# Kernel optimization log

Hardware: AMD Instinct MI355X
Metric: run time of the kernel (lower is better)

Reference implementation:

```python
import jax, jax.numpy as jnp
import numpy as np

NEG = -1e30  # log-space 'zero' sentinel (avoids -inf NaNs in grads)
BLANK = 0


def setup_inputs() -> dict:
    key = jax.random.key(0)
    k1, k2 = jax.random.split(key)
    B, T, V, L = 32, 1000, 1024, 100
    predictions = jax.random.normal(k1, (B, T, V), dtype=jnp.float32)
    prediction_lengths = jnp.full((B,), T, dtype=jnp.int32)
    # targets exclude the blank index (values in [1, V))
    ground_truths = jax.random.randint(k2, (B, L), 1, V, dtype=jnp.int32)
    ground_truth_lengths = jnp.full((B,), L, dtype=jnp.int32)
    return dict(predictions=predictions,
                prediction_lengths=prediction_lengths,
                ground_truths=ground_truths,
                ground_truth_lengths=ground_truth_lengths)


def _ctc_loss(log_probs, targets, input_lengths, target_lengths, blank):
    # log_probs: [T, B, V] (already log_softmaxed); targets: [B, L]
    T, B, V = log_probs.shape
    L = targets.shape[1]
    S = 2 * L + 1  # extended label seq with interleaved blanks
    s = jnp.arange(S)
    lab_idx = jnp.minimum(s // 2, L - 1)
    ext = jnp.where((s % 2 == 0)[None, :], blank, targets[:, lab_idx])  # [B, S]
    ext_m2 = jnp.pad(ext[:, :-2], ((0, 0), (2, 0)), constant_values=-1)
    skip = (s >= 2)[None, :] & (ext != blank) & (ext != ext_m2)  # allowed 2-step transition

    def end_ll(alpha):
        # logaddexp of alpha at positions 2*tl and 2*tl-1
        e1 = jnp.take_along_axis(alpha, (2 * target_lengths)[:, None], axis=1)[:, 0]
        e2 = jnp.take_along_axis(alpha, jnp.maximum(2 * target_lengths - 1, 0)[:, None], axis=1)[:, 0]
        return jnp.logaddexp(e1, e2)

    lp0 = jnp.take_along_axis(log_probs[0], ext, axis=1)  # [B, S]
    alpha0 = jnp.full((B, S), NEG, dtype=log_probs.dtype)
    alpha0 = alpha0.at[:, 0].set(lp0[:, 0])
    alpha0 = alpha0.at[:, 1].set(jnp.where(target_lengths > 0, lp0[:, 1], NEG))
    final0 = jnp.where(input_lengths == 1, end_ll(alpha0), NEG)

    def step(carry, inp):
        alpha, final = carry
        lp_t, t = inp
        lp_ext = jnp.take_along_axis(lp_t, ext, axis=1)  # [B, S]
        prev1 = jnp.pad(alpha[:, :-1], ((0, 0), (1, 0)), constant_values=NEG)
        prev2 = jnp.pad(alpha[:, :-2], ((0, 0), (2, 0)), constant_values=NEG)
        a = jnp.logaddexp(alpha, prev1)
        a = jnp.logaddexp(a, jnp.where(skip, prev2, NEG))
        new_alpha = a + lp_ext
        alpha = jnp.where((t < input_lengths)[:, None], new_alpha, alpha)
        final = jnp.where(t == input_lengths - 1, end_ll(alpha), final)
        return (alpha, final), None

    ts = jnp.arange(1, T)
    (_, final), _ = jax.lax.scan(step, (alpha0, final0), (log_probs[1:], ts))
    loss = -final
    loss = jnp.where(final <= NEG * 0.5, 0.0, loss)  # zero_infinity=True
    # torch reduction='mean': per-sample loss / target_length, then batch mean
    return jnp.mean(loss / target_lengths.astype(loss.dtype))


def reference(predictions, prediction_lengths, ground_truths, ground_truth_lengths):
    # [B, T, V] -> [T, B, V], then log_softmax over vocab
    log_probs = jax.nn.log_softmax(jnp.transpose(predictions, (1, 0, 2)), axis=2)
    return _ctc_loss(log_probs, ground_truths, prediction_lengths,
                     ground_truth_lengths, BLANK)
```

## Files before the change

### kernel.cpp

```cpp
#include <hip/hip_runtime.h>
#include <hip/hip_bf16.h>

#define DPPF(x, ctrl) \
    __int_as_float(__builtin_amdgcn_mov_dpp(__float_as_int(x), (ctrl), 0xf, 0xf, true))

__global__ void lse_gather_kernel(const float* __restrict__ pred,
                                  const int* __restrict__ tgt,
                                  float4* __restrict__ gat,
                                  float* __restrict__ out,
                                  int T, int V, int L, int nrows) {
    if (blockIdx.x == 0 && threadIdx.x == 0) out[0] = 0.0f;

    const int wid = blockIdx.x * (blockDim.x >> 6) + (threadIdx.x >> 6);
    if (wid >= nrows) return;
    const int lane = threadIdx.x & 63;
    const int b = wid / T;

    const float* row = pred + (size_t)wid * V;
    float4 w0 = ((const float4*)row)[lane];
    float4 w1 = ((const float4*)row)[lane + 64];
    float4 w2 = ((const float4*)row)[lane + 128];
    float4 w3 = ((const float4*)row)[lane + 192];

    float m = fmaxf(fmaxf(fmaxf(w0.x, w0.y), fmaxf(w0.z, w0.w)),
                    fmaxf(fmaxf(w1.x, w1.y), fmaxf(w1.z, w1.w)));
    m = fmaxf(m, fmaxf(fmaxf(w2.x, w2.y), fmaxf(w2.z, w2.w)));
    m = fmaxf(m, fmaxf(fmaxf(w3.x, w3.y), fmaxf(w3.z, w3.w)));
    #pragma unroll
    for (int off = 1; off < 64; off <<= 1) m = fmaxf(m, __shfl_xor(m, off, 64));

    float s = __expf(w0.x - m) + __expf(w0.y - m) + __expf(w0.z - m) + __expf(w0.w - m)
            + __expf(w1.x - m) + __expf(w1.y - m) + __expf(w1.z - m) + __expf(w1.w - m)
            + __expf(w2.x - m) + __expf(w2.y - m) + __expf(w2.z - m) + __expf(w2.w - m)
            + __expf(w3.x - m) + __expf(w3.y - m) + __expf(w3.z - m) + __expf(w3.w - m);
    #pragma unroll
    for (int off = 1; off < 64; off <<= 1) s += __shfl_xor(s, off, 64);

    const float lse = m + __logf(s);

    float pz = __expf(row[0] - lse);
    float px = 0.0f, py = 0.0f;
    const int l0 = 2 * lane, l1i = 2 * lane + 1;
    if (l0  < L) px = __expf(row[tgt[b * L + l0 ]] - lse);
    if (l1i < L) py = __expf(row[tgt[b * L + l1i]] - lse);

    float4 o; o.x = px; o.y = py; o.z = pz; o.w = 0.0f;
    gat[(size_t)wid * 64 + lane] = o;
}

__global__ __launch_bounds__(64, 1)
void ctc_alpha_wave(const float4* __restrict__ gat,
                    const int* __restrict__ tgt,
                    const int* __restrict__ in_len,
                    const int* __restrict__ tg_len,
                    float* __restrict__ out,
                    int T, int L, int B) {
    const int b = blockIdx.x;
    const int k = threadIdx.x;
    const int S = 2 * L + 1;

    const int il = in_len[b];
    const int tl = tg_len[b];
    const float4* gb = gat + (size_t)b * T * 64;

    const bool v1 = (4 * k + 1 < S);
    const bool v3 = (4 * k + 3 < S);
    bool sk1 = false, sk3 = false;
    if (v1 && k > 0) {
        int tc = tgt[b * L + 2 * k], tp = tgt[b * L + 2 * k - 1];
        sk1 = (tc != 0) && (tc != tp);
    }
    if (v3) {
        int tc = tgt[b * L + 2 * k + 1], tp = tgt[b * L + 2 * k];
        sk3 = (tc != 0) && (tc != tp);
    }

    float q0 = 0.0f, q1 = 0.0f, q2 = 0.0f, q3 = 0.0f;
    {
        float4 f0 = gb[k];
        if (k == 0) { q0 = f0.z; q1 = (tl > 0) ? f0.x : 0.0f; }
    }
    int acc = 0;

    const int tmax = (il < T) ? il : T;
    const int rmax = T - 1;

    float4 P[24];
    #pragma unroll
    for (int d = 0; d < 24; ++d) {
        int r = 1 + d; r = (r > rmax) ? rmax : r;
        P[d] = gb[(size_t)r * 64 + k];
    }

    int t = 1;

#define STEP(p)                                                              \
    {                                                                        \
        float qm = DPPF(q3, 0x138);           \
        qm = (k == 0) ? 0.0f : qm;                                           \
        float n0 = (q0 + qm) * (p).z;                                        \
        float n1 = (q1 + q0 + (sk1 ? qm : 0.0f)) * (p).x;                    \
        float n2 = (q2 + q1) * (p).z;                                        \
        float n3 = (q3 + q2 + (sk3 ? q1 : 0.0f)) * (p).y;                    \
        q0 = n0; q1 = n1; q2 = n2; q3 = n3;                                  \
        ++t;                                                                 \
    }

#define RENORM                                                               \
    {                                                                        \
        float mx = fmaxf(fmaxf(q0, q1), fmaxf(q2, q3));                      \
        mx = fmaxf(mx, DPPF(mx, 0x111));                     \
        mx = fmaxf(mx, DPPF(mx, 0x112));                     \
        mx = fmaxf(mx, DPPF(mx, 0x114));                     \
        mx = fmaxf(mx, DPPF(mx, 0x118));                     \
        mx = fmaxf(mx, DPPF(mx, 0x142));                   \
        mx = fmaxf(mx, DPPF(mx, 0x143));                   \
        int me = (__builtin_amdgcn_readlane(__float_as_int(mx), 63) >> 23) & 0xff; \
        float sc = __int_as_float(((me == 0) ? 127 : (254 - me)) << 23);     \
        acc += (me == 0) ? 0 : (me - 127);                                   \
        q0 *= sc; q1 *= sc; q2 *= sc; q3 *= sc;                              \
    }

    while (t + 24 <= tmax) {
        #pragma unroll
        for (int u = 0; u < 24; ++u) {
            float4 p = P[u];
            { int r = t + 24; r = (r > rmax) ? rmax : r;
              P[u] = gb[(size_t)r * 64 + k]; }
            STEP(p)
            if ((u & 3) == 3) RENORM
        }
    }
    while (t + 4 <= tmax) {
        { float4 pa = gb[(size_t)t * 64 + k]; STEP(pa) }
        { float4 pb = gb[(size_t)t * 64 + k]; STEP(pb) }
        { float4 pc = gb[(size_t)t * 64 + k]; STEP(pc) }
        { float4 pd = gb[(size_t)t * 64 + k]; STEP(pd) }
        RENORM
    }
    while (t < tmax) {
        float4 pr = gb[(size_t)t * 64 + k]; STEP(pr)
    }
#undef STEP
#undef RENORM

    const int e1 = 2 * tl;
    const int e2 = (2 * tl - 1 > 0) ? (2 * tl - 1) : 0;
    const int i1 = e1 & 3, l1 = e1 >> 2;
    const int i2 = e2 & 3, l2 = e2 >> 2;
    float m1 = (i1 == 0) ? q0 : (i1 == 1) ? q1 : (i1 == 2) ? q2 : q3;
    float m2 = (i2 == 0) ? q0 : (i2 == 1) ? q1 : (i2 == 2) ? q2 : q3;
    float ev1 = __shfl(m1, l1, 64);
    float ev2 = __shfl(m2, l2, 64);
    float qs = ev1 + ev2;

    if (k == 0) {
        float loss = 0.0f;
        if (qs > 0.0f && il >= 1 && il <= T) {
            float fin_log2 = (float)acc + log2f(qs);
            loss = -fin_log2 * 0.6931471805599453f;
        }
        atomicAdd(out, loss / ((float)tl * (float)B));
    }
}

extern "C" void kernel_launch(void* const* d_in, const int* in_sizes, int n_in,
                              void* d_out, int out_size, void* d_ws, size_t ws_size,
                              hipStream_t stream) {
    const float* pred = (const float*)d_in[0];
    const int*   plen = (const int*)d_in[1];
    const int*   gt   = (const int*)d_in[2];
    const int*   glen = (const int*)d_in[3];
    float* out = (float*)d_out;

    const int B = in_sizes[1];
    const int L = in_sizes[2] / B;
    const int V = 1024;
    const int T = in_sizes[0] / B / V;

    float4* gat = (float4*)d_ws;

    const int nrows = B * T;
    const int wavesPerBlk = 4;
    const int nblk = (nrows + wavesPerBlk - 1) / wavesPerBlk;
    lse_gather_kernel<<<nblk, 64 * wavesPerBlk, 0, stream>>>(
        pred, gt, gat, out, T, V, L, nrows);

    ctc_alpha_wave<<<B, 64, 0, stream>>>(gat, gt, plen, glen, out, T, L, B);
}
```

Before: 270.6 us.

## Stream alpha-recursion inputs through an LDS ring via direct global-to-LDS loads

Replaces the 24-entry register prefetch array in the CTC alpha kernel with a 32-slot LDS ring buffer. The ring is filled by asynchronous global_load_lds instructions running about 29 steps ahead, paced by explicit vmcnt waits, and only three rows are kept in registers. The aim is to cut register pressure and keep a deeper prefetch so the serial recurrence never stalls on memory latency. It depends on hand-counted vmcnt values matching the outstanding loads, which is fragile if the compiler emits other vector memory ops. Any rows left at the tail are read directly from global memory.

```diff
diff --git a/kernel.cpp b/kernel.cpp
--- a/kernel.cpp
+++ b/kernel.cpp
@@ -3,6 +3,12 @@
 
 #define DPPF(x, ctrl) \
     __int_as_float(__builtin_amdgcn_mov_dpp(__float_as_int(x), (ctrl), 0xf, 0xf, true))
+
+typedef __attribute__((address_space(1))) unsigned int u32_g;
+typedef __attribute__((address_space(3))) unsigned int u32_l;
+__device__ __forceinline__ void gload_lds16(const void* g, void* l) {
+    __builtin_amdgcn_global_load_lds((const u32_g*)g, (u32_l*)l, 16, 0, 0);
+}
 
 __global__ void lse_gather_kernel(const float* __restrict__ pred,
                                   const int* __restrict__ tgt,
@@ -55,6 +61,8 @@
                     const int* __restrict__ tg_len,
                     float* __restrict__ out,
                     int T, int L, int B) {
+    __shared__ float4 ring[32][64];
+
     const int b = blockIdx.x;
     const int k = threadIdx.x;
     const int S = 2 * L + 1;
@@ -85,12 +93,17 @@
     const int tmax = (il < T) ? il : T;
     const int rmax = T - 1;
 
-    float4 P[24];
+    asm volatile("s_waitcnt vmcnt(0)" ::: "memory");
+
     #pragma unroll
-    for (int d = 0; d < 24; ++d) {
-        int r = 1 + d; r = (r > rmax) ? rmax : r;
-        P[d] = gb[(size_t)r * 64 + k];
-    }
+    for (int d = 1; d <= 29; ++d) {
+        int r = (d > rmax) ? rmax : d;
+        gload_lds16(&gb[(size_t)r * 64 + k], &ring[r & 31][0]);
+    }
+    asm volatile("s_waitcnt vmcnt(26)" ::: "memory");
+    float4 pA = ring[1][k];
+    float4 pB = ring[2][k];
+    float4 pC = ring[3][k];
 
     int t = 1;
 
@@ -121,16 +134,20 @@
         q0 *= sc; q1 *= sc; q2 *= sc; q3 *= sc;                              \
     }
 
-    while (t + 24 <= tmax) {
+    while (t + 4 <= tmax && t + 32 <= rmax) {
         #pragma unroll
-        for (int u = 0; u < 24; ++u) {
-            float4 p = P[u];
-            { int r = t + 24; r = (r > rmax) ? rmax : r;
-              P[u] = gb[(size_t)r * 64 + k]; }
-            STEP(p)
-            if ((u & 3) == 3) RENORM
+        for (int u = 0; u < 4; ++u) {
+            asm volatile("s_waitcnt vmcnt(25)" ::: "memory");
+            float4 pN = ring[(t + 3) & 31][k];
+            gload_lds16(&gb[(size_t)(t + 29) * 64 + k], &ring[(t + 29) & 31][0]);
+            STEP(pA)
+            pA = pB; pB = pC; pC = pN;
         }
-    }
+        RENORM
+    }
+
+    asm volatile("s_waitcnt vmcnt(0)" ::: "memory");
+
     while (t + 4 <= tmax) {
         { float4 pa = gb[(size_t)t * 64 + k]; STEP(pa) }
         { float4 pb = gb[(size_t)t * 64 + k]; STEP(pb) }
```

After: 425.3 us. 57.2% more time.

## Add helper wave that prefetches gathered probabilities into cache ahead of alpha recursion

Applied to the files above, without the earlier changes.

Replaces the 24-deep register prefetch ring in the CTC alpha kernel with a second wavefront per block. The helper wave loads the next 16-step chunk of gathered probabilities to warm the cache, then synchronises with the compute wave after each chunk. The compute wave now issues plain loads just before each step and relies on those lines already being cached. This frees registers and shortens the compute loop, but adds a block barrier every 16 steps and makes each step's load latency depend on a cache hit rather than on registers already holding the data.

```diff
diff --git a/kernel.cpp b/kernel.cpp
--- a/kernel.cpp
+++ b/kernel.cpp
@@ -48,7 +48,7 @@
     gat[(size_t)wid * 64 + lane] = o;
 }
 
-__global__ __launch_bounds__(64, 1)
+__global__ __launch_bounds__(128, 1)
 void ctc_alpha_wave(const float4* __restrict__ gat,
                     const int* __restrict__ tgt,
                     const int* __restrict__ in_len,
@@ -56,12 +56,40 @@
                     float* __restrict__ out,
                     int T, int L, int B) {
     const int b = blockIdx.x;
-    const int k = threadIdx.x;
+    const int w = threadIdx.x >> 6;
+    const int k = threadIdx.x & 63;
     const int S = 2 * L + 1;
 
     const int il = in_len[b];
     const int tl = tg_len[b];
     const float4* gb = gat + (size_t)b * T * 64;
+
+    const int tmax = (il < T) ? il : T;
+    const int rmax = T - 1;
+    const int nsteps = tmax - 1;
+    const int nc = (nsteps >= 16) ? (nsteps >> 4) : 0;
+
+    if (w == 1) {
+        for (int c = 0; c < nc; ++c) {
+            const int base = 1 + 16 * (c + 1);
+            float4 f0, f1, f2, f3, f4, f5, f6, f7;
+            float4 f8, f9, fa, fb, fc, fd, fe, ff;
+#define PF(var, j) { int r = base + (j); r = (r > rmax) ? rmax : r;          \
+                     var = gb[(size_t)r * 64 + k]; }
+            PF(f0, 0)  PF(f1, 1)  PF(f2, 2)  PF(f3, 3)
+            PF(f4, 4)  PF(f5, 5)  PF(f6, 6)  PF(f7, 7)
+            PF(f8, 8)  PF(f9, 9)  PF(fa, 10) PF(fb, 11)
+            PF(fc, 12) PF(fd, 13) PF(fe, 14) PF(ff, 15)
+#undef PF
+            float keep = ((f0.x + f1.x) + (f2.x + f3.x))
+                       + ((f4.x + f5.x) + (f6.x + f7.x))
+                       + ((f8.x + f9.x) + (fa.x + fb.x))
+                       + ((fc.x + fd.x) + (fe.x + ff.x));
+            asm volatile("" :: "v"(keep));
+            __syncthreads();
+        }
+        return;
+    }
 
     const bool v1 = (4 * k + 1 < S);
     const bool v3 = (4 * k + 3 < S);
@@ -81,16 +109,6 @@
         if (k == 0) { q0 = f0.z; q1 = (tl > 0) ? f0.x : 0.0f; }
     }
     int acc = 0;
-
-    const int tmax = (il < T) ? il : T;
-    const int rmax = T - 1;
-
-    float4 P[24];
-    #pragma unroll
-    for (int d = 0; d < 24; ++d) {
-        int r = 1 + d; r = (r > rmax) ? rmax : r;
-        P[d] = gb[(size_t)r * 64 + k];
-    }
 
     int t = 1;
 
@@ -121,16 +139,18 @@
         q0 *= sc; q1 *= sc; q2 *= sc; q3 *= sc;                              \
     }
 
-    while (t + 24 <= tmax) {
+    for (int c = 0; c < nc; ++c) {
         #pragma unroll
-        for (int u = 0; u < 24; ++u) {
-            float4 p = P[u];
-            { int r = t + 24; r = (r > rmax) ? rmax : r;
-              P[u] = gb[(size_t)r * 64 + k]; }
-            STEP(p)
-            if ((u & 3) == 3) RENORM
+        for (int g = 0; g < 4; ++g) {
+            { float4 pa = gb[(size_t)t * 64 + k]; STEP(pa) }
+            { float4 pb = gb[(size_t)t * 64 + k]; STEP(pb) }
+            { float4 pc = gb[(size_t)t * 64 + k]; STEP(pc) }
+            { float4 pd = gb[(size_t)t * 64 + k]; STEP(pd) }
+            RENORM
         }
-    }
+        __syncthreads();
+    }
+
     while (t + 4 <= tmax) {
         { float4 pa = gb[(size_t)t * 64 + k]; STEP(pa) }
         { float4 pb = gb[(size_t)t * 64 + k]; STEP(pb) }
@@ -186,5 +206,5 @@
     lse_gather_kernel<<<nblk, 64 * wavesPerBlk, 0, stream>>>(
         pred, gt, gat, out, T, V, L, nrows);
 
-    ctc_alpha_wave<<<B, 64, 0, stream>>>(gat, gt, plen, glen, out, T, L, B);
+    ctc_alpha_wave<<<B, 128, 0, stream>>>(gat, gt, plen, glen, out, T, L, B);
 }
```

Result: faster. 251.6 us (-7.0%).
